# Kernel optimization log

Measured on AMD Instinct MI355X. Metric: run time of the kernel, lower is better.

Reference implementation:

```python
import jax, jax.numpy as jnp
import numpy as np

B, M, D, W = 4, 4096, 64, 128  # batch/heads, seq (m=n), head dim (k), nnz per row


def setup_inputs() -> dict:
    key = jax.random.key(0)
    kq, kk, kv, kc = jax.random.split(key, 4)
    q = jax.random.normal(kq, (B, M, D), dtype=jnp.float32)
    k = jax.random.normal(kk, (B, M, D), dtype=jnp.float32)
    v = jax.random.normal(kv, (B, M, D), dtype=jnp.float32)
    # CSR with uniform W nonzeros per row: row_offsets = arange(M+1)*W implicit,
    # column_indices flattened is [M*W]; stored here as [M, W].
    column_indices = jax.random.randint(kc, (M, W), 0, M).astype(jnp.int32)
    return {"q": q, "k": k, "v": v, "column_indices": column_indices}


def reference(q, k, v, column_indices):
    # SDDMM: logits[b,i,w] = <q[b,i,:], k[b, col[i,w], :]> at sparse positions only
    k_g = k[:, column_indices, :]                      # [B, M, W, D]
    logits = jnp.einsum('bmd,bmwd->bmw', q, k_g)       # sparse values per row
    # Sparse row-wise softmax (each CSR row has exactly W entries)
    weights = jax.nn.softmax(logits, axis=-1)          # [B, M, W]
    # SpMM: out[b,i,d] = sum_w weights[b,i,w] * v[b, col[i,w], d]
    v_g = v[:, column_indices, :]                      # [B, M, W, D]
    out = jnp.einsum('bmw,bmwd->bmd', weights, v_g)    # [B, M, D]
    return out
```

## Files before the change

### kernel.cpp

```cpp
#include <hip/hip_runtime.h>
#include <hip/hip_fp16.h>
#include <math.h>

constexpr int B = 4;
constexpr int M = 4096;
constexpr int D = 64;
constexpr int W = 128;
constexpr int NELEM = B * M * D;

typedef _Float16 h2_t __attribute__((ext_vector_type(2)));
typedef int      i4_t __attribute__((ext_vector_type(4)));

__global__ __launch_bounds__(256) void cvt_f32_f16_2(
    const float4* __restrict__ k, const float4* __restrict__ v,
    __half2* __restrict__ kh, __half2* __restrict__ vh, int n4) {
    int i = blockIdx.x * 256 + threadIdx.x;
    const float4* src;
    __half2* dst;
    if (i < n4) { src = k; dst = kh; }
    else        { src = v; dst = vh; i -= n4; if (i >= n4) return; }
    float4 f = src[i];
    dst[2 * i]     = __floats2half2_rn(f.x, f.y);
    dst[2 * i + 1] = __floats2half2_rn(f.z, f.w);
}

__global__ __launch_bounds__(256, 4) void sparse_attn_f16(
    const float* __restrict__ q,
    const __half* __restrict__ kh,
    const __half* __restrict__ vh,
    const int*   __restrict__ idx,
    float*       __restrict__ out)
{
    const int blk  = blockIdx.x;
    const int b    = blk & 3;
    const int mb   = (blk >> 2) * 4;
    const int t    = threadIdx.x;
    const int wave = t >> 6;
    const int lane = t & 63;
    const int ci   = lane & 7;
    const int r    = lane >> 3;
    const int m    = mb + wave;

    __shared__ int idx_s[4 * W];

    ((int2*)idx_s)[t] = ((const int2*)(idx + (size_t)mb * W))[t];

    const float* qrow = q + ((size_t)b * M + m) * D;
    const float4 qa = ((const float4*)qrow)[2 * ci];
    const float4 qb = ((const float4*)qrow)[2 * ci + 1];
    h2_t qh[4];
    qh[0] = (h2_t){(_Float16)qa.x, (_Float16)qa.y};
    qh[1] = (h2_t){(_Float16)qa.z, (_Float16)qa.w};
    qh[2] = (h2_t){(_Float16)qb.x, (_Float16)qb.y};
    qh[3] = (h2_t){(_Float16)qb.z, (_Float16)qb.w};

    __syncthreads();

    int voff[16];
    #pragma unroll
    for (int j = 0; j < 16; ++j)
        voff[j] = idx_s[wave * W + j * 8 + r] * (D * 2) + ci * 16;

    const char* kb = (const char*)(kh + (size_t)b * M * D);
    const char* vb = (const char*)(vh + (size_t)b * M * D);

    float larr[16];
    #pragma unroll
    for (int batch = 0; batch < 2; ++batch) {
        i4_t kreg[8];
        #pragma unroll
        for (int jj = 0; jj < 8; ++jj)
            kreg[jj] = *(const i4_t*)(kb + voff[batch * 8 + jj]);
        #pragma unroll
        for (int jj = 0; jj < 8; ++jj) {
            union { i4_t v; h2_t h[4]; } u;
            u.v = kreg[jj];
            float part = 0.f;
            part = __builtin_amdgcn_fdot2(u.h[0], qh[0], part, false);
            part = __builtin_amdgcn_fdot2(u.h[1], qh[1], part, false);
            part = __builtin_amdgcn_fdot2(u.h[2], qh[2], part, false);
            part = __builtin_amdgcn_fdot2(u.h[3], qh[3], part, false);
            part += __shfl_xor(part, 1);
            part += __shfl_xor(part, 2);
            part += __shfl_xor(part, 4);
            larr[batch * 8 + jj] = part;
        }
    }

    i4_t vreg0[8];
    #pragma unroll
    for (int jj = 0; jj < 8; ++jj)
        vreg0[jj] = *(const i4_t*)(vb + voff[jj]);

    float mx = larr[0];
    #pragma unroll
    for (int j = 1; j < 16; ++j) mx = fmaxf(mx, larr[j]);
    mx = fmaxf(mx, __shfl_xor(mx, 8));
    mx = fmaxf(mx, __shfl_xor(mx, 16));
    mx = fmaxf(mx, __shfl_xor(mx, 32));

    float sum = 0.f;
    #pragma unroll
    for (int j = 0; j < 16; ++j) { larr[j] = __expf(larr[j] - mx); sum += larr[j]; }
    sum += __shfl_xor(sum, 8);
    sum += __shfl_xor(sum, 16);
    sum += __shfl_xor(sum, 32);
    const float inv = 1.0f / sum;

    float acc[8] = {0, 0, 0, 0, 0, 0, 0, 0};
    i4_t vreg1[8];
    #pragma unroll
    for (int jj = 0; jj < 8; ++jj)
        vreg1[jj] = *(const i4_t*)(vb + voff[8 + jj]);

    #pragma unroll
    for (int jj = 0; jj < 8; ++jj) {
        const float p = larr[jj];
        union { i4_t v; h2_t h[4]; } u;
        u.v = vreg0[jj];
        #pragma unroll
        for (int c = 0; c < 4; ++c) {
            acc[2 * c]     += p * (float)u.h[c][0];
            acc[2 * c + 1] += p * (float)u.h[c][1];
        }
    }
    #pragma unroll
    for (int jj = 0; jj < 8; ++jj) {
        const float p = larr[8 + jj];
        union { i4_t v; h2_t h[4]; } u;
        u.v = vreg1[jj];
        #pragma unroll
        for (int c = 0; c < 4; ++c) {
            acc[2 * c]     += p * (float)u.h[c][0];
            acc[2 * c + 1] += p * (float)u.h[c][1];
        }
    }
    #pragma unroll
    for (int o = 8; o < 64; o <<= 1) {
        #pragma unroll
        for (int i = 0; i < 8; ++i) acc[i] += __shfl_xor(acc[i], o);
    }

    if (r == 0) {
        float4* orow = (float4*)(out + ((size_t)b * M + m) * D);
        orow[2 * ci]     = make_float4(acc[0] * inv, acc[1] * inv,
                                       acc[2] * inv, acc[3] * inv);
        orow[2 * ci + 1] = make_float4(acc[4] * inv, acc[5] * inv,
                                       acc[6] * inv, acc[7] * inv);
    }
}

__global__ __launch_bounds__(128) void sparse_attn_f32(
    const float* __restrict__ q,
    const float* __restrict__ k,
    const float* __restrict__ v,
    const int*   __restrict__ idx,
    float*       __restrict__ out)
{
    const int blk = blockIdx.x;
    const int b = blk & 3;
    const int m = blk >> 2;
    const int t = threadIdx.x;
    const int lane = t & 63;
    const int wave = t >> 6;
    const int ci = lane & 15;
    const int r  = lane >> 4;

    __shared__ int   idx_s[W];
    __shared__ float sc_s[W];
    __shared__ float red_s[4];
    __shared__ float4 opart_s[16];

    idx_s[t] = idx[m * W + t];
    const float4 qf = ((const float4*)(q + ((size_t)b * M + m) * D))[ci];
    __syncthreads();

    const float* kb = k + (size_t)b * M * D;
    const int wbase = wave * 64;

    #pragma unroll
    for (int j = 0; j < 16; ++j) {
        const int w = wbase + j * 4 + r;
        const float4 kv = ((const float4*)(kb + (size_t)idx_s[w] * D))[ci];
        float part = kv.x * qf.x + kv.y * qf.y + kv.z * qf.z + kv.w * qf.w;
        part += __shfl_xor(part, 1);
        part += __shfl_xor(part, 2);
        part += __shfl_xor(part, 4);
        part += __shfl_xor(part, 8);
        if (ci == 0) sc_s[w] = part;
    }
    __syncthreads();

    float logit = sc_s[t];
    float mx = logit;
    #pragma unroll
    for (int o = 1; o < 64; o <<= 1) mx = fmaxf(mx, __shfl_xor(mx, o));
    if (lane == 0) red_s[wave] = mx;
    __syncthreads();
    mx = fmaxf(red_s[0], red_s[1]);
    float e = __expf(logit - mx);
    float sm = e;
    #pragma unroll
    for (int o = 1; o < 64; o <<= 1) sm += __shfl_xor(sm, o);
    if (lane == 0) red_s[2 + wave] = sm;
    __syncthreads();
    const float inv_denom = 1.0f / (red_s[2] + red_s[3]);
    sc_s[t] = e * inv_denom;
    __syncthreads();

    const float* vb = v + (size_t)b * M * D;
    float4 acc = {0.f, 0.f, 0.f, 0.f};
    #pragma unroll
    for (int j = 0; j < 16; ++j) {
        const int w = wbase + j * 4 + r;
        const float p = sc_s[w];
        const float4 vv = ((const float4*)(vb + (size_t)idx_s[w] * D))[ci];
        acc.x += p * vv.x; acc.y += p * vv.y;
        acc.z += p * vv.z; acc.w += p * vv.w;
    }
    acc.x += __shfl_xor(acc.x, 16); acc.y += __shfl_xor(acc.y, 16);
    acc.z += __shfl_xor(acc.z, 16); acc.w += __shfl_xor(acc.w, 16);
    acc.x += __shfl_xor(acc.x, 32); acc.y += __shfl_xor(acc.y, 32);
    acc.z += __shfl_xor(acc.z, 32); acc.w += __shfl_xor(acc.w, 32);

    if (wave == 0 && r == 0) opart_s[ci] = acc;
    __syncthreads();
    if (wave == 1 && r == 0) {
        const float4 o0 = opart_s[ci];
        float4 res;
        res.x = o0.x + acc.x; res.y = o0.y + acc.y;
        res.z = o0.z + acc.z; res.w = o0.w + acc.w;
        ((float4*)(out + ((size_t)b * M + m) * D))[ci] = res;
    }
}

extern "C" void kernel_launch(void* const* d_in, const int* in_sizes, int n_in,
                              void* d_out, int out_size, void* d_ws, size_t ws_size,
                              hipStream_t stream) {
    const float* q = (const float*)d_in[0];
    const float* k = (const float*)d_in[1];
    const float* v = (const float*)d_in[2];
    const int* idx = (const int*)d_in[3];
    float* out = (float*)d_out;

    const size_t need = (size_t)2 * NELEM * sizeof(__half);
    if (ws_size >= need) {
        __half* kh = (__half*)d_ws;
        __half* vh = kh + NELEM;
        const int n4 = NELEM / 4;
        const int cblk = (2 * n4 + 255) / 256;
        cvt_f32_f16_2<<<cblk, 256, 0, stream>>>((const float4*)k, (const float4*)v,
                                                (__half2*)kh, (__half2*)vh, n4);
        sparse_attn_f16<<<B * M / 4, 256, 0, stream>>>(q, kh, vh, idx, out);
    } else {
        sparse_attn_f32<<<B * M, 128, 0, stream>>>(q, k, v, idx, out);
    }
}
```

Baseline: 93.03 us.

## Split each attention row across two waves with cross-wave softmax merge

Each block now handles two rows instead of four, and two waves share one row, each taking 64 of the 128 nonzeros. The waves exchange their partial max and sum through shared memory and rescale their partial outputs online-softmax style before one wave writes the result. All K and V gathers are issued up front instead of in batches, and the index list is read straight from global memory rather than staged in shared memory. The intent is more memory-level parallelism per wave and a shorter serial chain per row, at the cost of twice as many blocks, an extra barrier and some redundant exp work.

```diff
diff --git a/kernel.cpp b/kernel.cpp
--- a/kernel.cpp
+++ b/kernel.cpp
@@ -33,91 +33,93 @@
 {
     const int blk  = blockIdx.x;
     const int b    = blk & 3;
-    const int mb   = (blk >> 2) * 4;
+    const int mp   = blk >> 2;
     const int t    = threadIdx.x;
     const int wave = t >> 6;
     const int lane = t & 63;
     const int ci   = lane & 7;
     const int r    = lane >> 3;
-    const int m    = mb + wave;
-
-    __shared__ int idx_s[4 * W];
-
-    ((int2*)idx_s)[t] = ((const int2*)(idx + (size_t)mb * W))[t];
+    const int row  = wave >> 1;
+    const int half = wave & 1;
+    const int m    = mp * 2 + row;
+
+    __shared__ float mx_s[2][2];
+    __shared__ float sm_s[2][2];
+    __shared__ float accbuf[2][64];
 
     const float* qrow = q + ((size_t)b * M + m) * D;
     const float4 qa = ((const float4*)qrow)[2 * ci];
     const float4 qb = ((const float4*)qrow)[2 * ci + 1];
+
+    const int* irow = idx + (size_t)m * W + half * 64 + r;
+    int voff[8];
+    #pragma unroll
+    for (int j = 0; j < 8; ++j)
+        voff[j] = irow[j * 8] * (D * 2) + ci * 16;
+
     h2_t qh[4];
     qh[0] = (h2_t){(_Float16)qa.x, (_Float16)qa.y};
     qh[1] = (h2_t){(_Float16)qa.z, (_Float16)qa.w};
     qh[2] = (h2_t){(_Float16)qb.x, (_Float16)qb.y};
     qh[3] = (h2_t){(_Float16)qb.z, (_Float16)qb.w};
 
-    __syncthreads();
-
-    int voff[16];
-    #pragma unroll
-    for (int j = 0; j < 16; ++j)
-        voff[j] = idx_s[wave * W + j * 8 + r] * (D * 2) + ci * 16;
-
     const char* kb = (const char*)(kh + (size_t)b * M * D);
     const char* vb = (const char*)(vh + (size_t)b * M * D);
 
-    float larr[16];
-    #pragma unroll
-    for (int batch = 0; batch < 2; ++batch) {
-        i4_t kreg[8];
-        #pragma unroll
-        for (int jj = 0; jj < 8; ++jj)
-            kreg[jj] = *(const i4_t*)(kb + voff[batch * 8 + jj]);
-        #pragma unroll
-        for (int jj = 0; jj < 8; ++jj) {
-            union { i4_t v; h2_t h[4]; } u;
-            u.v = kreg[jj];
-            float part = 0.f;
-            part = __builtin_amdgcn_fdot2(u.h[0], qh[0], part, false);
-            part = __builtin_amdgcn_fdot2(u.h[1], qh[1], part, false);
-            part = __builtin_amdgcn_fdot2(u.h[2], qh[2], part, false);
-            part = __builtin_amdgcn_fdot2(u.h[3], qh[3], part, false);
-            part += __shfl_xor(part, 1);
-            part += __shfl_xor(part, 2);
-            part += __shfl_xor(part, 4);
-            larr[batch * 8 + jj] = part;
-        }
-    }
-
-    i4_t vreg0[8];
-    #pragma unroll
-    for (int jj = 0; jj < 8; ++jj)
-        vreg0[jj] = *(const i4_t*)(vb + voff[jj]);
+    i4_t kreg[8];
+    i4_t vreg[8];
+    #pragma unroll
+    for (int j = 0; j < 8; ++j)
+        kreg[j] = *(const i4_t*)(kb + voff[j]);
+    #pragma unroll
+    for (int j = 0; j < 8; ++j)
+        vreg[j] = *(const i4_t*)(vb + voff[j]);
+
+    float larr[8];
+    #pragma unroll
+    for (int j = 0; j < 8; ++j) {
+        union { i4_t v; h2_t h[4]; } u;
+        u.v = kreg[j];
+        float part = 0.f;
+        part = __builtin_amdgcn_fdot2(u.h[0], qh[0], part, false);
+        part = __builtin_amdgcn_fdot2(u.h[1], qh[1], part, false);
+        part = __builtin_amdgcn_fdot2(u.h[2], qh[2], part, false);
+        part = __builtin_amdgcn_fdot2(u.h[3], qh[3], part, false);
+        part += __shfl_xor(part, 1);
+        part += __shfl_xor(part, 2);
+        part += __shfl_xor(part, 4);
+        larr[j] = part;
+    }
 
     float mx = larr[0];
     #pragma unroll
-    for (int j = 1; j < 16; ++j) mx = fmaxf(mx, larr[j]);
+    for (int j = 1; j < 8; ++j) mx = fmaxf(mx, larr[j]);
     mx = fmaxf(mx, __shfl_xor(mx, 8));
     mx = fmaxf(mx, __shfl_xor(mx, 16));
     mx = fmaxf(mx, __shfl_xor(mx, 32));
 
     float sum = 0.f;
     #pragma unroll
-    for (int j = 0; j < 16; ++j) { larr[j] = __expf(larr[j] - mx); sum += larr[j]; }
+    for (int j = 0; j < 8; ++j) { larr[j] = __expf(larr[j] - mx); sum += larr[j]; }
     sum += __shfl_xor(sum, 8);
     sum += __shfl_xor(sum, 16);
     sum += __shfl_xor(sum, 32);
-    const float inv = 1.0f / sum;
+
+    if (lane == 0) { mx_s[row][half] = mx; sm_s[row][half] = sum; }
+    __syncthreads();
+
+    const float mo = mx_s[row][half ^ 1];
+    const float so = sm_s[row][half ^ 1];
+    const float Mg = fmaxf(mx, mo);
+    const float denom  = __expf(mx - Mg) * sum + __expf(mo - Mg) * so;
+    const float cscale = __expf(mx - Mg) / denom;
 
     float acc[8] = {0, 0, 0, 0, 0, 0, 0, 0};
-    i4_t vreg1[8];
-    #pragma unroll
-    for (int jj = 0; jj < 8; ++jj)
-        vreg1[jj] = *(const i4_t*)(vb + voff[8 + jj]);
-
-    #pragma unroll
-    for (int jj = 0; jj < 8; ++jj) {
-        const float p = larr[jj];
+    #pragma unroll
+    for (int j = 0; j < 8; ++j) {
+        const float p = larr[j];
         union { i4_t v; h2_t h[4]; } u;
-        u.v = vreg0[jj];
+        u.v = vreg[j];
         #pragma unroll
         for (int c = 0; c < 4; ++c) {
             acc[2 * c]     += p * (float)u.h[c][0];
@@ -125,28 +127,32 @@
         }
     }
     #pragma unroll
-    for (int jj = 0; jj < 8; ++jj) {
-        const float p = larr[8 + jj];
-        union { i4_t v; h2_t h[4]; } u;
-        u.v = vreg1[jj];
-        #pragma unroll
-        for (int c = 0; c < 4; ++c) {
-            acc[2 * c]     += p * (float)u.h[c][0];
-            acc[2 * c + 1] += p * (float)u.h[c][1];
-        }
-    }
-    #pragma unroll
     for (int o = 8; o < 64; o <<= 1) {
         #pragma unroll
         for (int i = 0; i < 8; ++i) acc[i] += __shfl_xor(acc[i], o);
     }
 
-    if (r == 0) {
+    if (half == 1 && r == 0) {
+        ((float4*)&accbuf[row][ci * 8])[0] =
+            make_float4(acc[0] * cscale, acc[1] * cscale,
+                        acc[2] * cscale, acc[3] * cscale);
+        ((float4*)&accbuf[row][ci * 8 + 4])[0] =
+            make_float4(acc[4] * cscale, acc[5] * cscale,
+                        acc[6] * cscale, acc[7] * cscale);
+    }
+    __syncthreads();
+    if (half == 0 && r == 0) {
+        const float4 p0 = ((const float4*)&accbuf[row][ci * 8])[0];
+        const float4 p1 = ((const float4*)&accbuf[row][ci * 8 + 4])[0];
         float4* orow = (float4*)(out + ((size_t)b * M + m) * D);
-        orow[2 * ci]     = make_float4(acc[0] * inv, acc[1] * inv,
-                                       acc[2] * inv, acc[3] * inv);
-        orow[2 * ci + 1] = make_float4(acc[4] * inv, acc[5] * inv,
-                                       acc[6] * inv, acc[7] * inv);
+        orow[2 * ci] = make_float4(acc[0] * cscale + p0.x,
+                                   acc[1] * cscale + p0.y,
+                                   acc[2] * cscale + p0.z,
+                                   acc[3] * cscale + p0.w);
+        orow[2 * ci + 1] = make_float4(acc[4] * cscale + p1.x,
+                                       acc[5] * cscale + p1.y,
+                                       acc[6] * cscale + p1.z,
+                                       acc[7] * cscale + p1.w);
     }
 }
 
@@ -251,7 +257,7 @@
         const int cblk = (2 * n4 + 255) / 256;
         cvt_f32_f16_2<<<cblk, 256, 0, stream>>>((const float4*)k, (const float4*)v,
                                                 (__half2*)kh, (__half2*)vh, n4);
-        sparse_attn_f16<<<B * M / 4, 256, 0, stream>>>(q, kh, vh, idx, out);
+        sparse_attn_f16<<<B * M / 2, 256, 0, stream>>>(q, kh, vh, idx, out);
     } else {
         sparse_attn_f32<<<B * M, 128, 0, stream>>>(q, k, v, idx, out);
     }
```

Measured after the change: 93.39 us. About the same (+0.4%).

## Stream K/V tiles through LDS with bucketed indices and online softmax

Applied to the files above, without the earlier changes.

Replaces the per-row random gather of K/V rows with a tiled scheme. A new pre-pass kernel buckets each row's column indices by 128-row K/V tile and records per-tile offsets. The main kernel then streams every K/V tile of the batch into double-buffered, swizzled LDS using global_load_lds, and each 8-lane group consumes the entries of its row that fall in the current tile. Softmax becomes an online softmax with lazy rescaling, so the separate max and sum passes go away. The aim is to swap scattered 128-byte global gathers for coalesced streaming loads. The cost is that every block reads the whole K/V for its batch, an extra kernel launch, barriers every tile with per-row load imbalance, and one 512-thread block per CU.

```diff
diff --git a/kernel.cpp b/kernel.cpp
--- a/kernel.cpp
+++ b/kernel.cpp
@@ -8,8 +8,15 @@
 constexpr int W = 128;
 constexpr int NELEM = B * M * D;
 
+constexpr int T  = 128;
+constexpr int NT = M / T;
+constexpr int RB = 64;
+
 typedef _Float16 h2_t __attribute__((ext_vector_type(2)));
 typedef int      i4_t __attribute__((ext_vector_type(4)));
+
+typedef __attribute__((address_space(1))) const void* gptr_t;
+typedef __attribute__((address_space(3))) void*       sptr_t;
 
 __global__ __launch_bounds__(256) void cvt_f32_f16_2(
     const float4* __restrict__ k, const float4* __restrict__ v,
@@ -24,30 +31,68 @@
     dst[2 * i + 1] = __floats2half2_rn(f.z, f.w);
 }
 
-__global__ __launch_bounds__(256, 4) void sparse_attn_f16(
+__global__ __launch_bounds__(256) void bucket_idx(
+    const int* __restrict__ idx, unsigned short* __restrict__ idx2,
+    int* __restrict__ off) {
+    const int m    = blockIdx.x * 4 + (threadIdx.x >> 6);
+    const int lane = threadIdx.x & 63;
+    const int* row = idx + (size_t)m * W;
+    const int j0 = row[lane], j1 = row[lane + 64];
+    const int b0 = j0 >> 7,   b1 = j1 >> 7;
+    unsigned short* o2 = idx2 + (size_t)m * W;
+    int* op = off + (size_t)m * (NT + 1);
+    const unsigned long long lt = (1ULL << lane) - 1ULL;
+    int base = 0;
+    for (int t = 0; t < NT; ++t) {
+        unsigned long long q0 = __ballot(b0 == t);
+        unsigned long long q1 = __ballot(b1 == t);
+        if (lane == 0) op[t] = base;
+        const int c0 = __popcll(q0);
+        if (b0 == t) o2[base + __popcll(q0 & lt)] = (unsigned short)j0;
+        if (b1 == t) o2[base + c0 + __popcll(q1 & lt)] = (unsigned short)j1;
+        base += c0 + __popcll(q1);
+    }
+    if (lane == 0) op[NT] = base;
+}
+
+__global__ __launch_bounds__(512, 2) void sparse_attn_tiled(
     const float* __restrict__ q,
     const __half* __restrict__ kh,
     const __half* __restrict__ vh,
-    const int*   __restrict__ idx,
-    float*       __restrict__ out)
+    const unsigned short* __restrict__ idx2,
+    const int* __restrict__ off,
+    float* __restrict__ out)
 {
     const int blk  = blockIdx.x;
     const int b    = blk & 3;
-    const int mb   = (blk >> 2) * 4;
-    const int t    = threadIdx.x;
-    const int wave = t >> 6;
-    const int lane = t & 63;
-    const int ci   = lane & 7;
-    const int r    = lane >> 3;
-    const int m    = mb + wave;
-
-    __shared__ int idx_s[4 * W];
-
-    ((int2*)idx_s)[t] = ((const int2*)(idx + (size_t)mb * W))[t];
-
-    const float* qrow = q + ((size_t)b * M + m) * D;
-    const float4 qa = ((const float4*)qrow)[2 * ci];
-    const float4 qb = ((const float4*)qrow)[2 * ci + 1];
+    const int mc   = blk >> 2;
+    const int tid  = threadIdx.x;
+    const int wave = tid >> 6;
+    const int lane = tid & 63;
+    const int g    = lane >> 3;
+    const int c    = lane & 7;
+    const int mi   = wave * 8 + g;
+    const int m    = mc * RB + mi;
+
+    __shared__ i4_t ktile[2][T][8];
+    __shared__ i4_t vtile[2][T][8];
+    __shared__ __align__(16) unsigned short idx2_s[RB * W];
+    __shared__ unsigned short off_s[RB][NT + 1];
+
+    {
+        const i4_t* src = (const i4_t*)(idx2 + (size_t)mc * RB * W);
+        i4_t* dst = (i4_t*)idx2_s;
+        dst[tid]       = src[tid];
+        dst[tid + 512] = src[tid + 512];
+        const int* os = off + (size_t)mc * RB * (NT + 1);
+        unsigned short* od = &off_s[0][0];
+        for (int i = tid; i < RB * (NT + 1); i += 512)
+            od[i] = (unsigned short)os[i];
+    }
+
+    const float* qrow = q + ((size_t)b * M + m) * D + c * 8;
+    const float4 qa = ((const float4*)qrow)[0];
+    const float4 qb = ((const float4*)qrow)[1];
     h2_t qh[4];
     qh[0] = (h2_t){(_Float16)qa.x, (_Float16)qa.y};
     qh[1] = (h2_t){(_Float16)qa.z, (_Float16)qa.w};
@@ -56,98 +101,90 @@
 
     __syncthreads();
 
-    int voff[16];
-    #pragma unroll
-    for (int j = 0; j < 16; ++j)
-        voff[j] = idx_s[wave * W + j * 8 + r] * (D * 2) + ci * 16;
-
     const char* kb = (const char*)(kh + (size_t)b * M * D);
     const char* vb = (const char*)(vh + (size_t)b * M * D);
 
-    float larr[16];
-    #pragma unroll
-    for (int batch = 0; batch < 2; ++batch) {
-        i4_t kreg[8];
-        #pragma unroll
-        for (int jj = 0; jj < 8; ++jj)
-            kreg[jj] = *(const i4_t*)(kb + voff[batch * 8 + jj]);
-        #pragma unroll
-        for (int jj = 0; jj < 8; ++jj) {
-            union { i4_t v; h2_t h[4]; } u;
-            u.v = kreg[jj];
+    const int lr8 = lane >> 3;
+    const int swz = ((lane & 7) ^ lr8) * 16;
+
+    auto stage = [&](int p, int t) {
+        const int r0 = wave * 16;
+        const size_t g0 = (size_t)t * T + r0;
+        __builtin_amdgcn_global_load_lds(
+            (gptr_t)(kb + (g0 + lr8) * 128 + swz),
+            (sptr_t)&ktile[p][r0][0], 16, 0, 0);
+        __builtin_amdgcn_global_load_lds(
+            (gptr_t)(kb + (g0 + 8 + lr8) * 128 + swz),
+            (sptr_t)&ktile[p][r0 + 8][0], 16, 0, 0);
+        __builtin_amdgcn_global_load_lds(
+            (gptr_t)(vb + (g0 + lr8) * 128 + swz),
+            (sptr_t)&vtile[p][r0][0], 16, 0, 0);
+        __builtin_amdgcn_global_load_lds(
+            (gptr_t)(vb + (g0 + 8 + lr8) * 128 + swz),
+            (sptr_t)&vtile[p][r0 + 8][0], 16, 0, 0);
+    };
+
+    float acc[8] = {0, 0, 0, 0, 0, 0, 0, 0};
+    float mrun = -1e30f;
+    float l = 0.f;
+
+    stage(0, 0);
+    stage(1, 1);
+
+    for (int t = 0; t < NT; ++t) {
+        const int p = t & 1;
+        if (t < NT - 1) asm volatile("s_waitcnt vmcnt(4)" ::: "memory");
+        else            asm volatile("s_waitcnt vmcnt(0)" ::: "memory");
+        __builtin_amdgcn_s_barrier();
+        asm volatile("" ::: "memory");
+
+        const int base = off_s[mi][t];
+        const int cnt  = off_s[mi][t + 1] - base;
+        const unsigned short* ip = &idx2_s[mi * W + base];
+        for (int e = 0; e < cnt; ++e) {
+            const int jj = ip[e];
+            const int lr = jj & (T - 1);
+            union { i4_t v; h2_t h[4]; } uk, uv;
+            uk.v = ktile[p][lr][c ^ (lr & 7)];
             float part = 0.f;
-            part = __builtin_amdgcn_fdot2(u.h[0], qh[0], part, false);
-            part = __builtin_amdgcn_fdot2(u.h[1], qh[1], part, false);
-            part = __builtin_amdgcn_fdot2(u.h[2], qh[2], part, false);
-            part = __builtin_amdgcn_fdot2(u.h[3], qh[3], part, false);
+            part = __builtin_amdgcn_fdot2(uk.h[0], qh[0], part, false);
+            part = __builtin_amdgcn_fdot2(uk.h[1], qh[1], part, false);
+            part = __builtin_amdgcn_fdot2(uk.h[2], qh[2], part, false);
+            part = __builtin_amdgcn_fdot2(uk.h[3], qh[3], part, false);
             part += __shfl_xor(part, 1);
             part += __shfl_xor(part, 2);
             part += __shfl_xor(part, 4);
-            larr[batch * 8 + jj] = part;
+            float d = part - mrun;
+            if (d > 8.0f) {
+                const float s = __expf(-d);
+                l *= s;
+                #pragma unroll
+                for (int i = 0; i < 8; ++i) acc[i] *= s;
+                mrun = part;
+                d = 0.f;
+            }
+            const float pw = __expf(d);
+            l += pw;
+            uv.v = vtile[p][lr][c ^ (lr & 7)];
+            #pragma unroll
+            for (int k2 = 0; k2 < 4; ++k2) {
+                acc[2 * k2]     += pw * (float)uv.h[k2][0];
+                acc[2 * k2 + 1] += pw * (float)uv.h[k2][1];
+            }
         }
-    }
-
-    i4_t vreg0[8];
-    #pragma unroll
-    for (int jj = 0; jj < 8; ++jj)
-        vreg0[jj] = *(const i4_t*)(vb + voff[jj]);
-
-    float mx = larr[0];
-    #pragma unroll
-    for (int j = 1; j < 16; ++j) mx = fmaxf(mx, larr[j]);
-    mx = fmaxf(mx, __shfl_xor(mx, 8));
-    mx = fmaxf(mx, __shfl_xor(mx, 16));
-    mx = fmaxf(mx, __shfl_xor(mx, 32));
-
-    float sum = 0.f;
-    #pragma unroll
-    for (int j = 0; j < 16; ++j) { larr[j] = __expf(larr[j] - mx); sum += larr[j]; }
-    sum += __shfl_xor(sum, 8);
-    sum += __shfl_xor(sum, 16);
-    sum += __shfl_xor(sum, 32);
-    const float inv = 1.0f / sum;
-
-    float acc[8] = {0, 0, 0, 0, 0, 0, 0, 0};
-    i4_t vreg1[8];
-    #pragma unroll
-    for (int jj = 0; jj < 8; ++jj)
-        vreg1[jj] = *(const i4_t*)(vb + voff[8 + jj]);
-
-    #pragma unroll
-    for (int jj = 0; jj < 8; ++jj) {
-        const float p = larr[jj];
-        union { i4_t v; h2_t h[4]; } u;
-        u.v = vreg0[jj];
-        #pragma unroll
-        for (int c = 0; c < 4; ++c) {
-            acc[2 * c]     += p * (float)u.h[c][0];
-            acc[2 * c + 1] += p * (float)u.h[c][1];
-        }
-    }
-    #pragma unroll
-    for (int jj = 0; jj < 8; ++jj) {
-        const float p = larr[8 + jj];
-        union { i4_t v; h2_t h[4]; } u;
-        u.v = vreg1[jj];
-        #pragma unroll
-        for (int c = 0; c < 4; ++c) {
-            acc[2 * c]     += p * (float)u.h[c][0];
-            acc[2 * c + 1] += p * (float)u.h[c][1];
-        }
-    }
-    #pragma unroll
-    for (int o = 8; o < 64; o <<= 1) {
-        #pragma unroll
-        for (int i = 0; i < 8; ++i) acc[i] += __shfl_xor(acc[i], o);
-    }
-
-    if (r == 0) {
-        float4* orow = (float4*)(out + ((size_t)b * M + m) * D);
-        orow[2 * ci]     = make_float4(acc[0] * inv, acc[1] * inv,
-                                       acc[2] * inv, acc[3] * inv);
-        orow[2 * ci + 1] = make_float4(acc[4] * inv, acc[5] * inv,
-                                       acc[6] * inv, acc[7] * inv);
-    }
+
+        asm volatile("s_waitcnt lgkmcnt(0)" ::: "memory");
+        __builtin_amdgcn_s_barrier();
+        asm volatile("" ::: "memory");
+        if (t + 2 < NT) stage(p, t + 2);
+    }
+
+    const float inv = 1.0f / l;
+    float* orow = out + ((size_t)b * M + m) * D + c * 8;
+    ((float4*)orow)[0] = make_float4(acc[0] * inv, acc[1] * inv,
+                                     acc[2] * inv, acc[3] * inv);
+    ((float4*)orow)[1] = make_float4(acc[4] * inv, acc[5] * inv,
+                                     acc[6] * inv, acc[7] * inv);
 }
 
 __global__ __launch_bounds__(128) void sparse_attn_f32(
@@ -243,15 +280,22 @@
     const int* idx = (const int*)d_in[3];
     float* out = (float*)d_out;
 
-    const size_t need = (size_t)2 * NELEM * sizeof(__half);
+    const size_t sz_kv   = (size_t)NELEM * sizeof(__half);
+    const size_t sz_idx2 = (size_t)M * W * sizeof(unsigned short);
+    const size_t sz_off  = (size_t)M * (NT + 1) * sizeof(int);
+    const size_t need = 2 * sz_kv + sz_idx2 + sz_off;
     if (ws_size >= need) {
-        __half* kh = (__half*)d_ws;
-        __half* vh = kh + NELEM;
+        __half* khp = (__half*)d_ws;
+        __half* vhp = khp + NELEM;
+        unsigned short* idx2 = (unsigned short*)((char*)d_ws + 2 * sz_kv);
+        int* off = (int*)((char*)d_ws + 2 * sz_kv + sz_idx2);
+
         const int n4 = NELEM / 4;
         const int cblk = (2 * n4 + 255) / 256;
         cvt_f32_f16_2<<<cblk, 256, 0, stream>>>((const float4*)k, (const float4*)v,
-                                                (__half2*)kh, (__half2*)vh, n4);
-        sparse_attn_f16<<<B * M / 4, 256, 0, stream>>>(q, kh, vh, idx, out);
+                                                (__half2*)khp, (__half2*)vhp, n4);
+        bucket_idx<<<M / 4, 256, 0, stream>>>(idx, idx2, off);
+        sparse_attn_tiled<<<B * M / RB, 512, 0, stream>>>(q, khp, vhp, idx2, off, out);
     } else {
         sparse_attn_f32<<<B * M, 128, 0, stream>>>(q, k, v, idx, out);
     }
```

After: 177.0 us. 1.9x slower.
